# Optimization experiments

Measured on AMD Instinct MI355X. Metric: run time of the kernel, lower is better.

Reference implementation:

```python
import jax, jax.numpy as jnp
import numpy as np

D_MODEL = 1024
D_STATE = 16
D_CONV = 4
EXPAND = 2
D_INNER = EXPAND * D_MODEL
BATCH = 4
SEQLEN = 2048
LN_EPS = 1e-5


def setup_inputs() -> dict:
    key = jax.random.key(0)
    ks = jax.random.split(key, 10)
    x = jax.random.normal(ks[0], (BATCH, SEQLEN, D_MODEL), dtype=jnp.float32)
    # parameters (torch Linear weights stored transposed here: [in, out])
    in_proj_w = jax.random.normal(ks[1], (D_MODEL, 2 * D_INNER), jnp.float32) * (1.0 / np.sqrt(D_MODEL))
    conv_w = jax.random.normal(ks[2], (D_INNER, 1, D_CONV), jnp.float32) * (1.0 / np.sqrt(D_CONV))  # OIH, depthwise
    conv_b = jax.random.normal(ks[3], (D_INNER,), jnp.float32) * 0.02
    x_proj_w = jax.random.normal(ks[4], (D_INNER, 2 * D_STATE), jnp.float32) * (1.0 / np.sqrt(D_INNER))
    dt_proj_w = jax.random.normal(ks[5], (D_INNER, D_INNER), jnp.float32) * (1.0 / np.sqrt(D_INNER))
    dt_proj_b = jax.random.normal(ks[6], (D_INNER,), jnp.float32) * 0.02
    # A = arange(1..d_state) repeated over d_inner; store log
    A_log = jnp.log(jnp.tile(jnp.arange(1, D_STATE + 1, dtype=jnp.float32)[None, :], (D_INNER, 1)))
    D_param = jnp.ones((D_INNER,), jnp.float32)
    out_proj_w = jax.random.normal(ks[7], (D_INNER, D_MODEL), jnp.float32) * (1.0 / np.sqrt(D_INNER))
    ln_gamma = jnp.ones((D_MODEL,), jnp.float32)
    ln_beta = jnp.zeros((D_MODEL,), jnp.float32)
    return {
        'x': x, 'ln_gamma': ln_gamma, 'ln_beta': ln_beta,
        'in_proj_w': in_proj_w, 'conv_w': conv_w, 'conv_b': conv_b,
        'x_proj_w': x_proj_w, 'dt_proj_w': dt_proj_w, 'dt_proj_b': dt_proj_b,
        'A_log': A_log, 'D_param': D_param, 'out_proj_w': out_proj_w,
    }


def _selective_scan(u, delta, A, Bm):
    # u, delta: [B, L, d_inner]; Bm: [B, L, d_state]; A: [d_inner, d_state]
    batch, _, d_inner = u.shape
    d_state = A.shape[1]

    def step(h, inp):
        u_t, d_t, b_t = inp  # [B,di], [B,di], [B,ds]
        dA = jnp.exp(d_t[..., None] * A)                      # [B,di,ds]
        h = h * dA + (u_t * d_t)[..., None] * b_t[:, None, :]  # [B,di,ds]
        return h, h.sum(-1)                                    # y_t: [B,di]

    h0 = jnp.zeros((batch, d_inner, d_state), u.dtype)
    xs = (jnp.swapaxes(u, 0, 1), jnp.swapaxes(delta, 0, 1), jnp.swapaxes(Bm, 0, 1))
    _, ys = jax.lax.scan(step, h0, xs)  # ys: [L,B,di]
    return jnp.swapaxes(ys, 0, 1)


def reference(x, ln_gamma, ln_beta, in_proj_w, conv_w, conv_b, x_proj_w,
              dt_proj_w, dt_proj_b, A_log, D_param, out_proj_w):
    residual = x
    # LayerNorm
    mu = x.mean(-1, keepdims=True)
    var = jnp.mean(jnp.square(x - mu), axis=-1, keepdims=True)
    xn = (x - mu) * jax.lax.rsqrt(var + LN_EPS) * ln_gamma + ln_beta
    # in_proj, split into u (ssm path) and z (gate)
    xz = xn @ in_proj_w                      # [B,L,2*di]
    u, z = jnp.split(xz, 2, axis=-1)
    # causal depthwise conv1d (torch pads d_conv-1 both sides then slices -> left-pad only)
    uc = jnp.swapaxes(u, 1, 2)               # [B,di,L]
    uc = jax.lax.conv_general_dilated(
        uc, conv_w, window_strides=(1,), padding=[(D_CONV - 1, 0)],
        dimension_numbers=('NCH', 'OIH', 'NCH'), feature_group_count=D_INNER,
    ) + conv_b[None, :, None]
    u = jax.nn.silu(jnp.swapaxes(uc, 1, 2))  # [B,L,di]
    # projections; note: first d_state chunk of x_dbl is discarded (overwritten by dt_proj)
    x_dbl = u @ x_proj_w                     # [B,L,2*ds]
    Bm = x_dbl[..., D_STATE:]
    delta = jax.nn.softplus(u @ dt_proj_w + dt_proj_b)
    A = -jnp.exp(A_log)
    y = _selective_scan(u, delta, A, Bm)
    y = y + u * D_param
    y = y * jax.nn.silu(z)
    return y @ out_proj_w + residual
```

## Files before the change

kernel.cpp:

```cpp
#include <hip/hip_runtime.h>

typedef unsigned short u16;
typedef unsigned int   u32;

#define D_MODEL 1024
#define D_INNER 2048
#define D_STATE 16
#define SEQLEN  2048
#define BATCH   4
#define NROWS   (BATCH*SEQLEN)
#define CHUNK   128
#define NCHUNK  (SEQLEN/CHUNK)

__device__ __forceinline__ float b2f(u16 v){
  union { u32 i; float f; } u; u.i = ((u32)v) << 16; return u.f;
}
__device__ __forceinline__ u16 f2b(float f){
  union { float f; u32 i; } u; u.f = f;
  u32 x = u.i;
  return (u16)((x + 0x7fffu + ((x >> 16) & 1u)) >> 16);
}
__device__ __forceinline__ float h2f(u16 v){
  _Float16 h; __builtin_memcpy(&h, &v, 2); return (float)h;
}
__device__ __forceinline__ u16 f2h(float f){
  _Float16 h = (_Float16)f; u16 v; __builtin_memcpy(&v, &h, 2); return v;
}

typedef __bf16 bf16x8 __attribute__((ext_vector_type(8)));
typedef float  f32x4  __attribute__((ext_vector_type(4)));

__device__ __forceinline__ void async16(u16* lds, const u16* g){
  __builtin_amdgcn_global_load_lds(
      (const __attribute__((address_space(1))) void*)g,
      (__attribute__((address_space(3))) void*)lds,
      16, 0, 0);
}

__global__ __launch_bounds__(256) void wcvt_t_kernel(
    const float* __restrict__ W, u16* __restrict__ Bt, int Kd, int Nd)
{
  __shared__ u16 tile[32][33];
  const int n0 = blockIdx.x*32, k0 = blockIdx.y*32;
  const int tx = threadIdx.x & 31, ty = threadIdx.x >> 5;
  #pragma unroll
  for (int i=0;i<32;i+=8)
    tile[ty+i][tx] = f2b(W[(size_t)(k0+ty+i)*Nd + n0+tx]);
  __syncthreads();
  #pragma unroll
  for (int i=0;i<32;i+=8)
    Bt[(size_t)(n0+ty+i)*Kd + k0+tx] = tile[tx][ty+i];
}

__global__ __launch_bounds__(256) void wxcvt_kernel(
    const float* __restrict__ Wx, u16* __restrict__ Wxt)
{
  const int k = blockIdx.x*256 + threadIdx.x;
  #pragma unroll
  for (int n=0;n<16;n++)
    Wxt[n*D_INNER + k] = f2b(Wx[(size_t)k*32 + 16 + n]);
}

__global__ __launch_bounds__(256) void ln_kernel(
    const float* __restrict__ x, const float* __restrict__ g,
    const float* __restrict__ be, u16* __restrict__ xn)
{
  const int row = blockIdx.x;
  const float* xr = x + (size_t)row * D_MODEL;
  const int tid = threadIdx.x;
  float v[4]; float s = 0.f, s2 = 0.f;
  #pragma unroll
  for (int j=0;j<4;j++){
    float f = xr[tid + 256*j];
    v[j] = f; s += f; s2 += f*f;
  }
  #pragma unroll
  for (int o=32;o>0;o>>=1){ s += __shfl_down(s,o); s2 += __shfl_down(s2,o); }
  __shared__ float sh[8];
  const int wave = tid>>6, lane = tid&63;
  if (lane==0){ sh[wave]=s; sh[4+wave]=s2; }
  __syncthreads();
  const float ts  = sh[0]+sh[1]+sh[2]+sh[3];
  const float ts2 = sh[4]+sh[5]+sh[6]+sh[7];
  const float mu  = ts * (1.f/D_MODEL);
  const float var = ts2 * (1.f/D_MODEL) - mu*mu;
  const float rstd = rsqrtf(var + 1e-5f);
  u16* xo = xn + (size_t)row * D_MODEL;
  #pragma unroll
  for (int j=0;j<4;j++){
    int i = tid + 256*j;
    xo[i] = f2b((v[j]-mu)*rstd * g[i] + be[i]);
  }
}

template<int EPI>
__global__ __launch_bounds__(512) void gemm256(
    const u16* __restrict__ A, const u16* __restrict__ Bt,
    const float* __restrict__ bias, const float* __restrict__ resid,
    void* __restrict__ outv, int M, int N, int K, int gx, int gy)
{
  __shared__ __align__(16) u16 As[4*8192];
  __shared__ __align__(16) u16 Bs[4*8192];
  const int tid  = threadIdx.x;
  const int wave = tid >> 6, lane = tid & 63;
  const int quad = lane >> 4, l16 = lane & 15;
  const int wm = wave >> 2, wn = wave & 3;

  const int lid = blockIdx.x;
  int bx, by;
  if ((gx & 7) == 0) {
    const int xcd = lid & 7, q = lid >> 3;
    const int cpx = gx >> 3;
    const int qd  = q / gy;
    bx = xcd*cpx + qd;
    by = q - qd*gy;
  } else {
    bx = lid / gy;
    by = lid - bx*gy;
  }
  const int m0 = by*256, n0 = bx*256;

  const int gl   = (tid & 3) ^ ((tid >> 3) & 3);
  const int srow = tid >> 2;
  const u16* sA0 = A  + (size_t)(m0 + srow)*K       + gl*8;
  const u16* sA1 = A  + (size_t)(m0 + 128 + srow)*K + gl*8;
  const u16* sB0 = Bt + (size_t)(n0 + srow)*K       + gl*8;
  const u16* sB1 = Bt + (size_t)(n0 + 128 + srow)*K + gl*8;
  u16* dA = As + wave*512;
  u16* dB = Bs + wave*512;

  const int swz = quad ^ ((l16 >> 1) & 3);
  const char* aBase = (const char*)As + (wm*128 + l16)*64 + swz*16;
  const char* bBase = (const char*)Bs + (wn*64  + l16)*64 + swz*16;

  f32x4 acc[8][4];
  #pragma unroll
  for (int i=0;i<8;i++)
    #pragma unroll
    for (int j=0;j<4;j++) acc[i][j] = (f32x4){0.f,0.f,0.f,0.f};

  const int KT = K >> 5;

  #pragma unroll
  for (int p=0;p<3;p++){
    const int ko = p*32;
    u16* da = dA + p*8192; u16* db = dB + p*8192;
    async16(da,        sA0 + ko);
    async16(da + 4096, sA1 + ko);
    async16(db,        sB0 + ko);
    async16(db + 4096, sB1 + ko);
  }
  asm volatile("s_waitcnt vmcnt(8)" ::: "memory");
  __builtin_amdgcn_s_barrier();
  __builtin_amdgcn_sched_barrier(0);

  for (int kt = 0; kt < KT; ++kt){
    const int c = kt & 3;
    const char* aT = aBase + c*16384;
    const char* bT = bBase + c*16384;

    bf16x8 af[4], bfr[4];
    #pragma unroll
    for (int mf=0;mf<4;mf++) af[mf]  = *(const bf16x8*)(aT + mf*1024);
    #pragma unroll
    for (int nf=0;nf<4;nf++) bfr[nf] = *(const bf16x8*)(bT + nf*1024);
    {
      int k3 = kt + 3; k3 = (k3 < KT) ? k3 : (KT-1);
      const int b3 = (kt + 3) & 3;
      const int ko = k3*32;
      u16* da = dA + b3*8192; u16* db = dB + b3*8192;
      async16(da,        sA0 + ko);
      async16(da + 4096, sA1 + ko);
      async16(db,        sB0 + ko);
      async16(db + 4096, sB1 + ko);
    }
    __builtin_amdgcn_s_barrier();
    asm volatile("s_waitcnt lgkmcnt(0)" ::: "memory");
    __builtin_amdgcn_sched_barrier(0);
    __builtin_amdgcn_s_setprio(1);
    #pragma unroll
    for (int mf=0;mf<4;mf++)
      #pragma unroll
      for (int nf=0;nf<4;nf++)
        acc[mf][nf] = __builtin_amdgcn_mfma_f32_16x16x32_bf16(af[mf], bfr[nf], acc[mf][nf], 0, 0, 0);
    __builtin_amdgcn_s_setprio(0);
    __builtin_amdgcn_s_barrier();

    bf16x8 ag[4];
    #pragma unroll
    for (int mf=0;mf<4;mf++) ag[mf] = *(const bf16x8*)(aT + (4+mf)*1024);
    __builtin_amdgcn_s_barrier();
    asm volatile("s_waitcnt lgkmcnt(0)" ::: "memory");
    __builtin_amdgcn_sched_barrier(0);
    __builtin_amdgcn_s_setprio(1);
    #pragma unroll
    for (int mf=0;mf<4;mf++)
      #pragma unroll
      for (int nf=0;nf<4;nf++)
        acc[4+mf][nf] = __builtin_amdgcn_mfma_f32_16x16x32_bf16(ag[mf], bfr[nf], acc[4+mf][nf], 0, 0, 0);
    __builtin_amdgcn_s_setprio(0);
    asm volatile("s_waitcnt vmcnt(8)" ::: "memory");
    __builtin_amdgcn_s_barrier();
    __builtin_amdgcn_sched_barrier(0);
  }

  #pragma unroll
  for (int mf=0; mf<8; mf++){
    #pragma unroll
    for (int nf=0; nf<4; nf++){
      const int col = n0 + wn*64 + nf*16 + l16;
      #pragma unroll
      for (int j=0;j<4;j++){
        const int row = m0 + wm*128 + mf*16 + quad*4 + j;
        float v = acc[mf][nf][j];
        if (EPI == 1) {
          v += bias[col];
          v = (v > 20.f) ? v : log1pf(__expf(v));
          ((u16*)outv)[(size_t)row*N + col] = f2h(v);
        } else if (EPI == 2) {
          v += resid[(size_t)row*N + col];
          ((float*)outv)[(size_t)row*N + col] = v;
        } else {
          ((u16*)outv)[(size_t)row*N + col] = f2b(v);
        }
      }
    }
  }
}

__global__ __launch_bounds__(256) void conv_silu_kernel(
    const u16* __restrict__ xz, const float* __restrict__ cw,
    const float* __restrict__ cb, u16* __restrict__ u)
{
  const int idx = blockIdx.x*256 + threadIdx.x;
  const int c0 = (idx & 255) * 8;
  const int bt = idx >> 8;
  const int t  = bt & (SEQLEN-1);
  float acc[8];
  #pragma unroll
  for (int j=0;j<8;j++) acc[j] = cb[c0+j];
  #pragma unroll
  for (int k=0;k<4;k++){
    if (t - 3 + k >= 0){
      bf16x8 xv = *reinterpret_cast<const bf16x8*>(xz + (size_t)(bt-3+k)*4096 + c0);
      #pragma unroll
      for (int j=0;j<8;j++)
        acc[j] = fmaf(cw[(c0+j)*4 + k], (float)xv[j], acc[j]);
    }
  }
  u16 o[8];
  #pragma unroll
  for (int j=0;j<8;j++){
    float sv = acc[j] / (1.f + __expf(-acc[j]));
    o[j] = f2b(sv);
  }
  __builtin_memcpy(u + (size_t)bt*D_INNER + c0, o, 16);
}

__global__ __launch_bounds__(256) void xproj_kernel(
    const u16* __restrict__ u, const u16* __restrict__ Wxt, float* __restrict__ Bm)
{
  const int wave = threadIdx.x >> 6, lane = threadIdx.x & 63;
  const int m = blockIdx.x*4 + wave;
  const int n = lane & 15, kq = lane >> 4;
  const u16* ur = u   + (size_t)m*D_INNER + kq*512;
  const u16* wr = Wxt + (size_t)n*D_INNER + kq*512;
  float acc = 0.f;
  #pragma unroll 4
  for (int i=0;i<512;i+=8){
    bf16x8 uv = *reinterpret_cast<const bf16x8*>(ur + i);
    bf16x8 wv = *reinterpret_cast<const bf16x8*>(wr + i);
    #pragma unroll
    for (int j=0;j<8;j++) acc = fmaf((float)uv[j], (float)wv[j], acc);
  }
  acc += __shfl_xor(acc, 16);
  acc += __shfl_xor(acc, 32);
  if (lane < 16) Bm[(size_t)m*16 + n] = acc;
}

__global__ __launch_bounds__(256) void scan_partial(
    const u16* __restrict__ uu, const u16* __restrict__ delta16,
    const float* __restrict__ Bm, const float* __restrict__ Alog,
    float* __restrict__ hend, float* __restrict__ sumdt)
{
  const int b = blockIdx.y, ch = blockIdx.z;
  const int c = blockIdx.x*256 + threadIdx.x;
  const int row0 = b*SEQLEN + ch*CHUNK;
  float A[16], h[16];
  #pragma unroll
  for (int s=0;s<16;s++){ A[s] = -__expf(Alog[c*16+s]); h[s]=0.f; }
  __shared__ float Bsh[CHUNK*16];
  const float* src = Bm + (size_t)row0*16;
  #pragma unroll
  for (int j=0;j<8;j++) Bsh[threadIdx.x + 256*j] = src[threadIdx.x + 256*j];
  __syncthreads();

  float S = 0.f;
  float dta[8], uva[8], dtb[8], uvb[8];
  #pragma unroll
  for (int j=0;j<8;j++){
    size_t r = (size_t)(row0+j);
    dta[j] = h2f(delta16[r*D_INNER+c]);
    uva[j] = b2f(uu[r*D_INNER+c]);
  }
  #pragma unroll 1
  for (int g=0; g<CHUNK; g+=16){
    #pragma unroll
    for (int j=0;j<8;j++){
      int tl = g+8+j; tl = tl < CHUNK ? tl : CHUNK-1;
      size_t r = (size_t)(row0+tl);
      dtb[j] = h2f(delta16[r*D_INNER+c]);
      uvb[j] = b2f(uu[r*D_INNER+c]);
    }
    #pragma unroll
    for (int j=0;j<8;j++){
      float dt=dta[j], uv=uva[j]; S += dt; float xv=dt*uv;
      const float* Bt = &Bsh[(g+j)*16];
      #pragma unroll
      for (int s=0;s<16;s++) h[s] = fmaf(h[s], __expf(dt*A[s]), xv*Bt[s]);
    }
    #pragma unroll
    for (int j=0;j<8;j++){
      int tl = g+16+j; tl = tl < CHUNK ? tl : CHUNK-1;
      size_t r = (size_t)(row0+tl);
      dta[j] = h2f(delta16[r*D_INNER+c]);
      uva[j] = b2f(uu[r*D_INNER+c]);
    }
    #pragma unroll
    for (int j=0;j<8;j++){
      float dt=dtb[j], uv=uvb[j]; S += dt; float xv=dt*uv;
      const float* Bt = &Bsh[(g+8+j)*16];
      #pragma unroll
      for (int s=0;s<16;s++) h[s] = fmaf(h[s], __expf(dt*A[s]), xv*Bt[s]);
    }
  }
  const size_t base = ((size_t)(b*NCHUNK+ch)*16)*D_INNER + c;
  #pragma unroll
  for (int s=0;s<16;s++) hend[base + (size_t)s*D_INNER] = h[s];
  sumdt[(size_t)(b*NCHUNK+ch)*D_INNER + c] = S;
}

__global__ __launch_bounds__(256) void scan_combine(
    const float* __restrict__ hend, const float* __restrict__ sumdt,
    const float* __restrict__ Alog, float* __restrict__ hin)
{
  const int b = blockIdx.y;
  const int c = blockIdx.x*256 + threadIdx.x;
  float A[16], h[16];
  #pragma unroll
  for (int s=0;s<16;s++){ A[s] = -__expf(Alog[c*16+s]); h[s]=0.f; }
  #pragma unroll 1
  for (int k=0;k<NCHUNK;k++){
    const size_t base = ((size_t)(b*NCHUNK+k)*16)*D_INNER + c;
    #pragma unroll
    for (int s=0;s<16;s++) hin[base + (size_t)s*D_INNER] = h[s];
    const float S = sumdt[(size_t)(b*NCHUNK+k)*D_INNER + c];
    #pragma unroll
    for (int s=0;s<16;s++)
      h[s] = fmaf(h[s], __expf(S*A[s]), hend[base + (size_t)s*D_INNER]);
  }
}

__global__ __launch_bounds__(256) void scan_final(
    const u16* __restrict__ uu, const u16* __restrict__ delta16,
    const float* __restrict__ Bm, const u16* __restrict__ xz,
    const float* __restrict__ Alog, const float* __restrict__ Dpar,
    const float* __restrict__ hin, u16* __restrict__ yg)
{
  const int b = blockIdx.y, ch = blockIdx.z;
  const int c = blockIdx.x*256 + threadIdx.x;
  const int row0 = b*SEQLEN + ch*CHUNK;
  float A[16], h[16];
  const size_t base = ((size_t)(b*NCHUNK+ch)*16)*D_INNER + c;
  #pragma unroll
  for (int s=0;s<16;s++){
    A[s] = -__expf(Alog[c*16+s]);
    h[s] = hin[base + (size_t)s*D_INNER];
  }
  const float Dc = Dpar[c];
  __shared__ float Bsh[CHUNK*16];
  const float* src = Bm + (size_t)row0*16;
  #pragma unroll
  for (int j=0;j<8;j++) Bsh[threadIdx.x + 256*j] = src[threadIdx.x + 256*j];
  __syncthreads();

  float dta[8], uva[8], zva[8], dtb[8], uvb[8], zvb[8];
  #pragma unroll
  for (int j=0;j<8;j++){
    size_t r = (size_t)(row0+j);
    dta[j] = h2f(delta16[r*D_INNER+c]);
    uva[j] = b2f(uu[r*D_INNER+c]);
    zva[j] = b2f(xz[r*4096 + D_INNER + c]);
  }
  #pragma unroll 1
  for (int g=0; g<CHUNK; g+=16){
    #pragma unroll
    for (int j=0;j<8;j++){
      int tl = g+8+j; tl = tl < CHUNK ? tl : CHUNK-1;
      size_t r = (size_t)(row0+tl);
      dtb[j] = h2f(delta16[r*D_INNER+c]);
      uvb[j] = b2f(uu[r*D_INNER+c]);
      zvb[j] = b2f(xz[r*4096 + D_INNER + c]);
    }
    #pragma unroll
    for (int j=0;j<8;j++){
      float dt=dta[j], uv=uva[j], zv=zva[j];
      float xv=dt*uv, y=0.f;
      const float* Bt = &Bsh[(g+j)*16];
      #pragma unroll
      for (int s=0;s<16;s++){
        h[s] = fmaf(h[s], __expf(dt*A[s]), xv*Bt[s]);
        y += h[s];
      }
      y = fmaf(uv, Dc, y);
      float gz = zv/(1.f+__expf(-zv));
      yg[(size_t)(row0+g+j)*D_INNER + c] = f2b(y*gz);
    }
    #pragma unroll
    for (int j=0;j<8;j++){
      int tl = g+16+j; tl = tl < CHUNK ? tl : CHUNK-1;
      size_t r = (size_t)(row0+tl);
      dta[j] = h2f(delta16[r*D_INNER+c]);
      uva[j] = b2f(uu[r*D_INNER+c]);
      zva[j] = b2f(xz[r*4096 + D_INNER + c]);
    }
    #pragma unroll
    for (int j=0;j<8;j++){
      float dt=dtb[j], uv=uvb[j], zv=zvb[j];
      float xv=dt*uv, y=0.f;
      const float* Bt = &Bsh[(g+8+j)*16];
      #pragma unroll
      for (int s=0;s<16;s++){
        h[s] = fmaf(h[s], __expf(dt*A[s]), xv*Bt[s]);
        y += h[s];
      }
      y = fmaf(uv, Dc, y);
      float gz = zv/(1.f+__expf(-zv));
      yg[(size_t)(row0+g+8+j)*D_INNER + c] = f2b(y*gz);
    }
  }
}

extern "C" void kernel_launch(void* const* d_in, const int* in_sizes, int n_in,
                              void* d_out, int out_size, void* d_ws, size_t ws_size,
                              hipStream_t stream)
{
  const float* x    = (const float*)d_in[0];
  const float* lng  = (const float*)d_in[1];
  const float* lnb  = (const float*)d_in[2];
  const float* W1   = (const float*)d_in[3];
  const float* cw   = (const float*)d_in[4];
  const float* cb   = (const float*)d_in[5];
  const float* Wx   = (const float*)d_in[6];
  const float* Wdt  = (const float*)d_in[7];
  const float* dtb  = (const float*)d_in[8];
  const float* Alog = (const float*)d_in[9];
  const float* Dpar = (const float*)d_in[10];
  const float* Wout = (const float*)d_in[11];

  char* ws = (char*)d_ws;
  u16*   dlt   = (u16*)(ws);
  u16*   xn    = (u16*)(ws);
  u16*   xz    = (u16*)(ws + (32llu<<20));
  u16*   uu    = (u16*)(ws + (96llu<<20));
  float* Bm    = (float*)(ws + (128llu<<20));
  u16*   W1t   = (u16*)(ws + (129llu<<20));
  u16*   Wdtt  = (u16*)(ws + (137llu<<20));
  u16*   Woutt = (u16*)(ws + (145llu<<20));
  u16*   yg    = (u16*)(ws + (149llu<<20));
  float* hend  = (float*)(ws + (181llu<<20));
  float* sumdt = (float*)(ws + (189llu<<20));
  float* hin   = (float*)(ws + (190llu<<20));
  u16*   Wxt   = (u16*)(ws + (198llu<<20));

  wcvt_t_kernel<<<dim3(2*D_INNER/32, D_MODEL/32), 256, 0, stream>>>(W1,  W1t,  D_MODEL, 2*D_INNER);
  wcvt_t_kernel<<<dim3(D_INNER/32,  D_INNER/32), 256, 0, stream>>>(Wdt, Wdtt, D_INNER, D_INNER);
  wcvt_t_kernel<<<dim3(D_MODEL/32,  D_INNER/32), 256, 0, stream>>>(Wout,Woutt,D_INNER, D_MODEL);
  wxcvt_kernel<<<D_INNER/256, 256, 0, stream>>>(Wx, Wxt);

  ln_kernel<<<NROWS, 256, 0, stream>>>(x, lng, lnb, xn);

  {
    const int gx = 2*D_INNER/256, gy = NROWS/256;
    gemm256<0><<<gx*gy, 512, 0, stream>>>(
        xn, W1t, nullptr, nullptr, (void*)xz, NROWS, 2*D_INNER, D_MODEL, gx, gy);
  }

  conv_silu_kernel<<<(NROWS*D_INNER/8)/256, 256, 0, stream>>>(xz, cw, cb, uu);

  xproj_kernel<<<NROWS/4, 256, 0, stream>>>(uu, Wxt, Bm);

  {
    const int gx = D_INNER/256, gy = NROWS/256;
    gemm256<1><<<gx*gy, 512, 0, stream>>>(
        uu, Wdtt, dtb, nullptr, (void*)dlt, NROWS, D_INNER, D_INNER, gx, gy);
  }

  scan_partial<<<dim3(D_INNER/256, BATCH, NCHUNK), 256, 0, stream>>>(
      uu, dlt, Bm, Alog, hend, sumdt);
  scan_combine<<<dim3(D_INNER/256, BATCH), 256, 0, stream>>>(
      hend, sumdt, Alog, hin);
  scan_final<<<dim3(D_INNER/256, BATCH, NCHUNK), 256, 0, stream>>>(
      uu, dlt, Bm, xz, Alog, Dpar, hin, yg);

  {
    const int gx = D_MODEL/256, gy = NROWS/256;
    gemm256<2><<<gx*gy, 512, 0, stream>>>(
        yg, Woutt, nullptr, x, d_out, NROWS, D_MODEL, D_INNER, gx, gy);
  }

  (void)in_sizes; (void)n_in; (void)out_size; (void)ws_size;
}
```

Before: 777.5 us.

## Restructure GEMM pipeline to 64-wide K double-buffering with templated M tile

The bf16 MFMA GEMM moves from a 4-deep ring of 32-wide K slices to a 2-deep double buffer of 64-wide K steps. Async global-to-LDS copies for the next step are spread across the sub-phases of the current step's MFMA work, with matching vmcnt waits. A template parameter sets the M tile, and out_proj now uses 128-row tiles so that GEMM launches twice as many blocks. Launch bounds now request 2 blocks per CU. The tighter buffering and register limits may cost latency hiding or cause spills.

```diff
diff --git a/kernel.cpp b/kernel.cpp
--- a/kernel.cpp
+++ b/kernel.cpp
@@ -93,14 +93,23 @@
   }
 }
 
-template<int EPI>
-__global__ __launch_bounds__(512) void gemm256(
+template<int EPI, int MF>
+__global__ __launch_bounds__(512, 2) void gemm256(
     const u16* __restrict__ A, const u16* __restrict__ Bt,
     const float* __restrict__ bias, const float* __restrict__ resid,
     void* __restrict__ outv, int M, int N, int K, int gx, int gy)
 {
-  __shared__ __align__(16) u16 As[4*8192];
-  __shared__ __align__(16) u16 Bs[4*8192];
+  constexpr int BM     = MF*32;
+  constexpr int AKS_E  = BM*32;
+  constexpr int ABUF_E = 2*AKS_E;
+  constexpr int ABUF_B = ABUF_E*2;
+  constexpr int AKS_B  = AKS_E*2;
+  constexpr int CH     = (MF==8) ? 8 : 6;
+  constexpr int STG    = CH/(MF/2);
+
+  __shared__ __align__(16) u16 As[2*ABUF_E];
+  __shared__ __align__(16) u16 Bs[2*2*8192];
+
   const int tid  = threadIdx.x;
   const int wave = tid >> 6, lane = tid & 63;
   const int quad = lane >> 4, l16 = lane & 15;
@@ -118,100 +127,111 @@
     bx = lid / gy;
     by = lid - bx*gy;
   }
-  const int m0 = by*256, n0 = bx*256;
+  const int m0 = by*BM, n0 = bx*256;
 
   const int gl   = (tid & 3) ^ ((tid >> 3) & 3);
   const int srow = tid >> 2;
-  const u16* sA0 = A  + (size_t)(m0 + srow)*K       + gl*8;
-  const u16* sA1 = A  + (size_t)(m0 + 128 + srow)*K + gl*8;
-  const u16* sB0 = Bt + (size_t)(n0 + srow)*K       + gl*8;
-  const u16* sB1 = Bt + (size_t)(n0 + 128 + srow)*K + gl*8;
-  u16* dA = As + wave*512;
-  u16* dB = Bs + wave*512;
+  const u16* pA = A  + (size_t)(m0 + srow)*K + gl*8;
+  const u16* pB = Bt + (size_t)(n0 + srow)*K + gl*8;
+
+  auto STAGE = [&](int id, int kt2, int c2){
+    const size_t ko = (size_t)kt2*64;
+    if constexpr (MF == 8) {
+      const int s = id >> 2, rh = id & 1;
+      if ((id & 2) == 0)
+        async16(As + (c2*2+s)*AKS_E + rh*4096 + wave*512,
+                pA + (size_t)rh*128*K + ko + s*32);
+      else
+        async16(Bs + (c2*2+s)*8192 + rh*4096 + wave*512,
+                pB + (size_t)rh*128*K + ko + s*32);
+    } else {
+      const int s = id/3, r = id - s*3;
+      if (r == 0)
+        async16(As + (c2*2+s)*AKS_E + wave*512, pA + ko + s*32);
+      else
+        async16(Bs + (c2*2+s)*8192 + (r-1)*4096 + wave*512,
+                pB + (size_t)(r-1)*128*K + ko + s*32);
+    }
+  };
 
   const int swz = quad ^ ((l16 >> 1) & 3);
-  const char* aBase = (const char*)As + (wm*128 + l16)*64 + swz*16;
-  const char* bBase = (const char*)Bs + (wn*64  + l16)*64 + swz*16;
-
-  f32x4 acc[8][4];
-  #pragma unroll
-  for (int i=0;i<8;i++)
+  const char* aB = (const char*)As + (wm*(MF*16) + l16)*64 + swz*16;
+  const char* bB = (const char*)Bs + (wn*64      + l16)*64 + swz*16;
+
+  f32x4 acc[MF][4];
+  #pragma unroll
+  for (int i=0;i<MF;i++)
     #pragma unroll
     for (int j=0;j<4;j++) acc[i][j] = (f32x4){0.f,0.f,0.f,0.f};
 
-  const int KT = K >> 5;
-
-  #pragma unroll
-  for (int p=0;p<3;p++){
-    const int ko = p*32;
-    u16* da = dA + p*8192; u16* db = dB + p*8192;
-    async16(da,        sA0 + ko);
-    async16(da + 4096, sA1 + ko);
-    async16(db,        sB0 + ko);
-    async16(db + 4096, sB1 + ko);
-  }
-  asm volatile("s_waitcnt vmcnt(8)" ::: "memory");
+  const int KT = K >> 6;
+
+  #pragma unroll
+  for (int id=0; id<CH; ++id) STAGE(id, 0, 0);
+  if constexpr (MF==8) asm volatile("s_waitcnt vmcnt(4)" ::: "memory");
+  else                 asm volatile("s_waitcnt vmcnt(3)" ::: "memory");
   __builtin_amdgcn_s_barrier();
   __builtin_amdgcn_sched_barrier(0);
 
+  bf16x8 bfr[2][4];
+
   for (int kt = 0; kt < KT; ++kt){
-    const int c = kt & 3;
-    const char* aT = aBase + c*16384;
-    const char* bT = bBase + c*16384;
-
-    bf16x8 af[4], bfr[4];
-    #pragma unroll
-    for (int mf=0;mf<4;mf++) af[mf]  = *(const bf16x8*)(aT + mf*1024);
-    #pragma unroll
-    for (int nf=0;nf<4;nf++) bfr[nf] = *(const bf16x8*)(bT + nf*1024);
-    {
-      int k3 = kt + 3; k3 = (k3 < KT) ? k3 : (KT-1);
-      const int b3 = (kt + 3) & 3;
-      const int ko = k3*32;
-      u16* da = dA + b3*8192; u16* db = dB + b3*8192;
-      async16(da,        sA0 + ko);
-      async16(da + 4096, sA1 + ko);
-      async16(db,        sB0 + ko);
-      async16(db + 4096, sB1 + ko);
-    }
-    __builtin_amdgcn_s_barrier();
-    asm volatile("s_waitcnt lgkmcnt(0)" ::: "memory");
-    __builtin_amdgcn_sched_barrier(0);
-    __builtin_amdgcn_s_setprio(1);
-    #pragma unroll
-    for (int mf=0;mf<4;mf++)
-      #pragma unroll
-      for (int nf=0;nf<4;nf++)
-        acc[mf][nf] = __builtin_amdgcn_mfma_f32_16x16x32_bf16(af[mf], bfr[nf], acc[mf][nf], 0, 0, 0);
-    __builtin_amdgcn_s_setprio(0);
-    __builtin_amdgcn_s_barrier();
-
-    bf16x8 ag[4];
-    #pragma unroll
-    for (int mf=0;mf<4;mf++) ag[mf] = *(const bf16x8*)(aT + (4+mf)*1024);
-    __builtin_amdgcn_s_barrier();
-    asm volatile("s_waitcnt lgkmcnt(0)" ::: "memory");
-    __builtin_amdgcn_sched_barrier(0);
-    __builtin_amdgcn_s_setprio(1);
-    #pragma unroll
-    for (int mf=0;mf<4;mf++)
-      #pragma unroll
-      for (int nf=0;nf<4;nf++)
-        acc[4+mf][nf] = __builtin_amdgcn_mfma_f32_16x16x32_bf16(ag[mf], bfr[nf], acc[4+mf][nf], 0, 0, 0);
-    __builtin_amdgcn_s_setprio(0);
-    asm volatile("s_waitcnt vmcnt(8)" ::: "memory");
-    __builtin_amdgcn_s_barrier();
-    __builtin_amdgcn_sched_barrier(0);
-  }
-
-  #pragma unroll
-  for (int mf=0; mf<8; mf++){
+    const int c   = kt & 1;
+    const int kt2 = (kt+1 < KT) ? kt+1 : KT-1;
+    const int c2  = (kt+1) & 1;
+    const char* aT = aB + c*ABUF_B;
+    const char* bT = bB + c*32768;
+
+    #pragma unroll
+    for (int p = 0; p < MF/2; ++p){
+      const int ks = p & 1;
+      const int mg = (p >> 1) * 4;
+
+      bf16x8 af[4];
+      #pragma unroll
+      for (int i=0;i<4;i++)
+        af[i] = *(const bf16x8*)(aT + ks*AKS_B + (mg+i)*1024);
+      if (p < 2) {
+        #pragma unroll
+        for (int nf=0;nf<4;nf++)
+          bfr[ks][nf] = *(const bf16x8*)(bT + ks*16384 + nf*1024);
+      }
+
+      #pragma unroll
+      for (int i=0;i<STG;i++) STAGE(p*STG+i, kt2, c2);
+
+      if (p == 0) {
+        if constexpr (MF==8) asm volatile("s_waitcnt vmcnt(2)" ::: "memory");
+        else                 asm volatile("s_waitcnt vmcnt(3)" ::: "memory");
+      }
+      if (p == MF/2 - 1) {
+        if constexpr (MF==8) asm volatile("s_waitcnt vmcnt(4)" ::: "memory");
+        else                 asm volatile("s_waitcnt vmcnt(3)" ::: "memory");
+      }
+      __builtin_amdgcn_s_barrier();
+      asm volatile("s_waitcnt lgkmcnt(0)" ::: "memory");
+      __builtin_amdgcn_sched_barrier(0);
+      __builtin_amdgcn_s_setprio(1);
+      #pragma unroll
+      for (int mf=0;mf<4;mf++)
+        #pragma unroll
+        for (int nf=0;nf<4;nf++)
+          acc[mg+mf][nf] = __builtin_amdgcn_mfma_f32_16x16x32_bf16(
+              af[mf], bfr[ks][nf], acc[mg+mf][nf], 0, 0, 0);
+      __builtin_amdgcn_s_setprio(0);
+      __builtin_amdgcn_s_barrier();
+    }
+  }
+  asm volatile("s_waitcnt vmcnt(0)" ::: "memory");
+
+  #pragma unroll
+  for (int mf=0; mf<MF; mf++){
     #pragma unroll
     for (int nf=0; nf<4; nf++){
       const int col = n0 + wn*64 + nf*16 + l16;
       #pragma unroll
       for (int j=0;j<4;j++){
-        const int row = m0 + wm*128 + mf*16 + quad*4 + j;
+        const int row = m0 + wm*(MF*16) + mf*16 + quad*4 + j;
         float v = acc[mf][nf][j];
         if (EPI == 1) {
           v += bias[col];
@@ -482,7 +502,7 @@
 
   {
     const int gx = 2*D_INNER/256, gy = NROWS/256;
-    gemm256<0><<<gx*gy, 512, 0, stream>>>(
+    gemm256<0,8><<<gx*gy, 512, 0, stream>>>(
         xn, W1t, nullptr, nullptr, (void*)xz, NROWS, 2*D_INNER, D_MODEL, gx, gy);
   }
 
@@ -492,7 +512,7 @@
 
   {
     const int gx = D_INNER/256, gy = NROWS/256;
-    gemm256<1><<<gx*gy, 512, 0, stream>>>(
+    gemm256<1,8><<<gx*gy, 512, 0, stream>>>(
         uu, Wdtt, dtb, nullptr, (void*)dlt, NROWS, D_INNER, D_INNER, gx, gy);
   }
 
@@ -504,8 +524,8 @@
       uu, dlt, Bm, xz, Alog, Dpar, hin, yg);
 
   {
-    const int gx = D_MODEL/256, gy = NROWS/256;
-    gemm256<2><<<gx*gy, 512, 0, stream>>>(
+    const int gx = D_MODEL/256, gy = NROWS/128;
+    gemm256<2,4><<<gx*gy, 512, 0, stream>>>(
         yg, Woutt, nullptr, x, d_out, NROWS, D_MODEL, D_INNER, gx, gy);
   }
 
```

New measurement: 974.3 us. +25.3%, slower.
